# Performance work log

Hardware: AMD Instinct MI355X
Metric: run time of the kernel (lower is better)

The kernel has to match this reference:

```python
import jax, jax.numpy as jnp
import numpy as np

B, S, D, L = 64, 512, 256, 3
NUM_BUCKETS = 1500  # RelativePositionBias default


def _ln(x, g, b):
    m = x.mean(-1, keepdims=True)
    v = x.var(-1, keepdims=True)
    return (x - m) * jax.lax.rsqrt(v + 1e-5) * g + b


def setup_inputs() -> dict:
    key = jax.random.key(0)
    ks = jax.random.split(key, 10)
    s = 0.02
    f32 = jnp.float32
    return dict(
        x=jax.random.normal(ks[0], (B, S, D), f32),
        mask=jnp.ones((B, S), jnp.int32),
        bias_table=jax.random.normal(ks[1], (NUM_BUCKETS,), f32) * s,  # n_heads=1
        ln_g=jnp.ones((L, D), f32), ln_b=jnp.zeros((L, D), f32),
        wq=jax.random.normal(ks[2], (L, D, D), f32) * s, bq=jnp.zeros((L, D), f32),
        wk=jax.random.normal(ks[3], (L, D, D), f32) * s, bk=jnp.zeros((L, D), f32),
        wv=jax.random.normal(ks[4], (L, D, D), f32) * s, bv=jnp.zeros((L, D), f32),
        wo=jax.random.normal(ks[5], (L, D, D), f32) * s, bo=jnp.zeros((L, D), f32),
        cm_ln_g=jnp.ones((L, D), f32), cm_ln_b=jnp.zeros((L, D), f32),
        w1=jax.random.normal(ks[6], (L, D, D), f32) * s, b1=jnp.zeros((L, D), f32),
        w2=jax.random.normal(ks[7], (L, D, D), f32) * s, b2=jnp.zeros((L, D), f32),
    )


def reference(x, mask, bias_table, ln_g, ln_b, wq, bq, wk, bk, wv, bv, wo, bo,
              cm_ln_g, cm_ln_b, w1, b1, w2, b2):
    slen = x.shape[1]
    # relative position bias (RelativePositionBias.compute_bias), n_heads=1
    pos = jnp.arange(slen)
    rel = pos[None, :] - pos[:, None]        # memory - context
    maxn = slen - 1                          # torch.max(rel)
    bucket = jnp.where(rel < 0, -rel + maxn, rel)
    cp = bias_table[bucket]                  # [S, S], broadcasts over batch
    scale = jnp.sqrt(jnp.asarray(x.shape[-1], x.dtype))  # sqrt(hid_dim // 1)
    pad = (mask == 0)[:, None, :]            # [B, 1, S] key-side padding mask
    neg = jnp.finfo(x.dtype).min
    for j in range(L):
        h = _ln(x, ln_g[j], ln_b[j])
        q = h @ wq[j] + bq[j]
        k = h @ wk[j] + bk[j]
        v = h @ wv[j] + bv[j]
        e = jnp.einsum('bqd,bkd->bqk', q, k) / scale + cp
        e = jnp.where(pad, neg, e)
        a = jax.nn.softmax(e, axis=-1)
        o = jnp.einsum('bqk,bkd->bqd', a, v) @ wo[j] + bo[j]
        x = h + _ln(o, ln_g[j], ln_b[j])     # same LayerNorm reused, per source
        c = _ln(x, cm_ln_g[j], cm_ln_b[j])
        x = x + (jax.nn.gelu(c @ w1[j] + b1[j], approximate=False) @ w2[j] + b2[j])
    return x
```

## Files before the change

kernel.cpp:

```cpp
#include <hip/hip_runtime.h>
#include <hip/hip_bf16.h>
#include <math.h>

#define D_HID 256
#define N_B   64
#define S_LEN 512
#define N_L   3
#define M_ROWS (N_B * S_LEN)

typedef __bf16 bf16_t;
typedef __bf16 bf16x8 __attribute__((ext_vector_type(8)));
typedef __bf16 bf16x4 __attribute__((ext_vector_type(4)));
typedef float  f32x4  __attribute__((ext_vector_type(4)));
typedef unsigned int u32;

__device__ __forceinline__ f32x4 mfma16(bf16x8 a, bf16x8 b, f32x4 c) {
    return __builtin_amdgcn_mfma_f32_16x16x32_bf16(a, b, c, 0, 0, 0);
}

__device__ __forceinline__ void gld_lds16(const void* g, void* l) {
    __builtin_amdgcn_global_load_lds((const __attribute__((address_space(1))) u32*)g,
                                     (__attribute__((address_space(3))) u32*)l, 16, 0, 0);
}

__global__ __launch_bounds__(256) void transpose_w(const float* __restrict__ w,
                                                   bf16_t* __restrict__ wt,
                                                   int layer_stride) {
    int i = blockIdx.x * 256 + threadIdx.x;
    int k = i & 255;
    int n = (i >> 8) & 255;
    int l = i >> 16;
    wt[(size_t)l * layer_stride + n * 256 + k] =
        (bf16_t)w[((size_t)l << 16) + ((size_t)k << 8) + n];
}

__global__ __launch_bounds__(256) void ln_fwd(const float* __restrict__ in,
                                              const float* __restrict__ g,
                                              const float* __restrict__ b,
                                              float* __restrict__ H,
                                              bf16_t* __restrict__ Hb) {
    int row  = blockIdx.x * 4 + (threadIdx.x >> 6);
    int lane = threadIdx.x & 63;
    float4 x = ((const float4*)(in + (size_t)row * D_HID))[lane];
    float s  = x.x + x.y + x.z + x.w;
    float sq = x.x * x.x + x.y * x.y + x.z * x.z + x.w * x.w;
#pragma unroll
    for (int o = 1; o < 64; o <<= 1) { s += __shfl_xor(s, o); sq += __shfl_xor(sq, o); }
    float mean = s * (1.f / D_HID);
    float rstd = rsqrtf(sq * (1.f / D_HID) - mean * mean + 1e-5f);
    float4 gv = ((const float4*)g)[lane];
    float4 bv = ((const float4*)b)[lane];
    float4 h;
    h.x = (x.x - mean) * rstd * gv.x + bv.x;
    h.y = (x.y - mean) * rstd * gv.y + bv.y;
    h.z = (x.z - mean) * rstd * gv.z + bv.z;
    h.w = (x.w - mean) * rstd * gv.w + bv.w;
    ((float4*)(H + (size_t)row * D_HID))[lane] = h;
    bf16x4 hb = { (bf16_t)h.x, (bf16_t)h.y, (bf16_t)h.z, (bf16_t)h.w };
    *((bf16x4*)(Hb + (size_t)row * D_HID) + lane) = hb;
}

__global__ __launch_bounds__(256) void ln_res_ln(const float* __restrict__ T,
                                                 const float* __restrict__ H,
                                                 const float* __restrict__ g,
                                                 const float* __restrict__ b,
                                                 const float* __restrict__ cg,
                                                 const float* __restrict__ cb,
                                                 float* __restrict__ X,
                                                 bf16_t* __restrict__ Cb) {
    int row  = blockIdx.x * 4 + (threadIdx.x >> 6);
    int lane = threadIdx.x & 63;
    float4 t = ((const float4*)(T + (size_t)row * D_HID))[lane];
    float s  = t.x + t.y + t.z + t.w;
    float sq = t.x * t.x + t.y * t.y + t.z * t.z + t.w * t.w;
#pragma unroll
    for (int o = 1; o < 64; o <<= 1) { s += __shfl_xor(s, o); sq += __shfl_xor(sq, o); }
    float mean = s * (1.f / D_HID);
    float rstd = rsqrtf(sq * (1.f / D_HID) - mean * mean + 1e-5f);
    float4 gv = ((const float4*)g)[lane];
    float4 bv = ((const float4*)b)[lane];
    float4 hh = ((const float4*)(H + (size_t)row * D_HID))[lane];
    float4 x;
    x.x = hh.x + (t.x - mean) * rstd * gv.x + bv.x;
    x.y = hh.y + (t.y - mean) * rstd * gv.y + bv.y;
    x.z = hh.z + (t.z - mean) * rstd * gv.z + bv.z;
    x.w = hh.w + (t.w - mean) * rstd * gv.w + bv.w;
    ((float4*)(X + (size_t)row * D_HID))[lane] = x;
    float s2  = x.x + x.y + x.z + x.w;
    float sq2 = x.x * x.x + x.y * x.y + x.z * x.z + x.w * x.w;
#pragma unroll
    for (int o = 1; o < 64; o <<= 1) { s2 += __shfl_xor(s2, o); sq2 += __shfl_xor(sq2, o); }
    float mean2 = s2 * (1.f / D_HID);
    float rstd2 = rsqrtf(sq2 * (1.f / D_HID) - mean2 * mean2 + 1e-5f);
    float4 cgv = ((const float4*)cg)[lane];
    float4 cbv = ((const float4*)cb)[lane];
    bf16x4 c = { (bf16_t)((x.x - mean2) * rstd2 * cgv.x + cbv.x),
                 (bf16_t)((x.y - mean2) * rstd2 * cgv.y + cbv.y),
                 (bf16_t)((x.z - mean2) * rstd2 * cgv.z + cbv.z),
                 (bf16_t)((x.w - mean2) * rstd2 * cgv.w + cbv.w) };
    *((bf16x4*)(Cb + (size_t)row * D_HID) + lane) = c;
}

__device__ __forceinline__ void gemm_core(const bf16_t* __restrict__ A,
                                          const bf16_t* __restrict__ W,
                                          int m0, int n0,
                                          bf16_t* As, bf16_t* Bs,
                                          f32x4 (&acc)[4][4]) {
    const int tid  = threadIdx.x;
    const int lane = tid & 63;
    const int wid  = tid >> 6;
    const int wm = wid >> 1, wn = wid & 1;
    const int r = lane & 15, g = lane >> 4;
#pragma unroll 1
    for (int kt = 0; kt < 4; ++kt) {
        if (kt) __syncthreads();
#pragma unroll
        for (int i = 0; i < 4; ++i) {
            const int base8 = i * 256 + wid * 64;
            const int idx8  = base8 + lane;
            const int row   = idx8 >> 3;
            const int sc8   = (idx8 & 7) ^ (row & 7);
            gld_lds16(A + (size_t)(m0 + row) * D_HID + kt * 64 + sc8 * 8, As + base8 * 8);
            gld_lds16(W + (size_t)(n0 + row) * D_HID + kt * 64 + sc8 * 8, Bs + base8 * 8);
        }
        __syncthreads();
#pragma unroll
        for (int ks = 0; ks < 2; ++ks) {
            bf16x8 af[4], bfr[4];
#pragma unroll
            for (int mt = 0; mt < 4; ++mt) {
                const int row = wm * 64 + mt * 16 + r;
                const int c8  = (ks * 4 + g) ^ (row & 7);
                af[mt] = *(const bf16x8*)(As + row * 64 + c8 * 8);
            }
#pragma unroll
            for (int nt = 0; nt < 4; ++nt) {
                const int row = wn * 64 + nt * 16 + r;
                const int c8  = (ks * 4 + g) ^ (row & 7);
                bfr[nt] = *(const bf16x8*)(Bs + row * 64 + c8 * 8);
            }
#pragma unroll
            for (int mt = 0; mt < 4; ++mt)
#pragma unroll
                for (int nt = 0; nt < 4; ++nt)
                    acc[mt][nt] = mfma16(af[mt], bfr[nt], acc[mt][nt]);
        }
    }
}

__global__ __launch_bounds__(256) void gemm_qkv(const bf16_t* __restrict__ A,
                                                const bf16_t* __restrict__ Wp,
                                                const float* __restrict__ bq,
                                                const float* __restrict__ bk,
                                                const float* __restrict__ bv,
                                                bf16_t* __restrict__ Qb,
                                                bf16_t* __restrict__ Kb,
                                                bf16_t* __restrict__ Vt) {
    __shared__ bf16_t As[128 * 64], Bs[128 * 64];
    f32x4 acc[4][4] = {};
    const int m0 = blockIdx.x * 128, n0 = blockIdx.y * 128;
    gemm_core(A, Wp, m0, n0, As, Bs, acc);
    const int lane = threadIdx.x & 63, wid = threadIdx.x >> 6;
    const int wm = wid >> 1, wn = wid & 1, r = lane & 15, g = lane >> 4;
#pragma unroll
    for (int nt = 0; nt < 4; ++nt) {
        const int col = n0 + wn * 64 + nt * 16 + r;
        const int t = col >> 8, cc = col & 255;
        const float bias = (t == 0 ? bq : t == 1 ? bk : bv)[cc];
#pragma unroll
        for (int mt = 0; mt < 4; ++mt)
#pragma unroll
            for (int rr = 0; rr < 4; ++rr) {
                const int row = m0 + wm * 64 + mt * 16 + g * 4 + rr;
                const float v = acc[mt][nt][rr] + bias;
                if (t == 0)      Qb[(size_t)row * D_HID + cc] = (bf16_t)v;
                else if (t == 1) Kb[(size_t)row * D_HID + cc] = (bf16_t)v;
                else             Vt[((size_t)(row >> 9) * D_HID + cc) * S_LEN + (row & 511)] = (bf16_t)v;
            }
    }
}

template <int EPI>
__global__ __launch_bounds__(256) void gemm_one(const bf16_t* __restrict__ A,
                                                const bf16_t* __restrict__ W,
                                                const float* __restrict__ bias,
                                                void* __restrict__ outp,
                                                const float* __restrict__ addsrc) {
    __shared__ bf16_t As[128 * 64], Bs[128 * 64];
    f32x4 acc[4][4] = {};
    const int m0 = blockIdx.x * 128, n0 = blockIdx.y * 128;
    gemm_core(A, W, m0, n0, As, Bs, acc);
    const int lane = threadIdx.x & 63, wid = threadIdx.x >> 6;
    const int wm = wid >> 1, wn = wid & 1, r = lane & 15, g = lane >> 4;
#pragma unroll
    for (int nt = 0; nt < 4; ++nt) {
        const int col = n0 + wn * 64 + nt * 16 + r;
        const float bv = bias[col];
#pragma unroll
        for (int mt = 0; mt < 4; ++mt)
#pragma unroll
            for (int rr = 0; rr < 4; ++rr) {
                const size_t idx = (size_t)(m0 + wm * 64 + mt * 16 + g * 4 + rr) * D_HID + col;
                float v = acc[mt][nt][rr] + bv;
                if constexpr (EPI == 1) {
                    v = 0.5f * v * (1.f + erff(v * 0.70710678118654752f));
                    ((bf16_t*)outp)[idx] = (bf16_t)v;
                } else if constexpr (EPI == 2) {
                    ((float*)outp)[idx] = v;
                } else {
                    ((float*)outp)[idx] = addsrc[idx] + v;
                }
            }
    }
}

__global__ __launch_bounds__(256) void attn_fwd(const bf16_t* __restrict__ Q,
                                                const bf16_t* __restrict__ K,
                                                const bf16_t* __restrict__ Vt,
                                                const float* __restrict__ btab,
                                                const int* __restrict__ mask,
                                                bf16_t* __restrict__ AO) {
    const int b  = blockIdx.x;
    const int q0 = blockIdx.y * 32;
    const int tid  = threadIdx.x;
    const int lane = tid & 63;
    const int w    = tid >> 6;
    const int r = lane & 15, g = lane >> 4;

    __shared__ float  s_tile[32][65];
    __shared__ bf16_t p_tile[32][72];
    __shared__ float  m_s[32], l_s[32], fac_s[32];
    if (tid < 32) { m_s[tid] = -3.0e38f; l_s[tid] = 0.f; }

    const bf16_t* Qp  = Q  + ((size_t)b * S_LEN + q0) * D_HID;
    const bf16_t* Kp  = K  + (size_t)b * S_LEN * D_HID;
    const bf16_t* Vtp = Vt + (size_t)b * D_HID * S_LEN;

    f32x4 oacc[2][4] = {};

    for (int kt = 0; kt < 8; ++kt) {
        const int k0 = kt * 64;
        f32x4 sacc0 = {0.f, 0.f, 0.f, 0.f}, sacc1 = {0.f, 0.f, 0.f, 0.f};
#pragma unroll
        for (int ks = 0; ks < 8; ++ks) {
            const int kb = ks * 32 + g * 8;
            bf16x8 aq0 = *(const bf16x8*)(Qp + (size_t)r * D_HID + kb);
            bf16x8 aq1 = *(const bf16x8*)(Qp + (size_t)(16 + r) * D_HID + kb);
            bf16x8 bk  = *(const bf16x8*)(Kp + (size_t)(k0 + w * 16 + r) * D_HID + kb);
            sacc0 = mfma16(aq0, bk, sacc0);
            sacc1 = mfma16(aq1, bk, sacc1);
        }
#pragma unroll
        for (int rr = 0; rr < 4; ++rr) {
            s_tile[g * 4 + rr][w * 16 + r]      = sacc0[rr];
            s_tile[16 + g * 4 + rr][w * 16 + r] = sacc1[rr];
        }
        __syncthreads();
        {
            const int q  = tid >> 3;
            const int kc = (tid & 7) * 8;
            const int qg = q0 + q;
            const int4 mk0 = *(const int4*)(mask + b * S_LEN + k0 + kc);
            const int4 mk1 = *(const int4*)(mask + b * S_LEN + k0 + kc + 4);
            const int mk[8] = { mk0.x, mk0.y, mk0.z, mk0.w, mk1.x, mk1.y, mk1.z, mk1.w };
            float e[8];
#pragma unroll
            for (int i = 0; i < 8; ++i) {
                const int kk = k0 + kc + i;
                const int rel = kk - qg;
                const int bucket = (rel < 0) ? (511 - rel) : rel;
                float ev = s_tile[q][kc + i] * 0.0625f + btab[bucket];
                if (mk[i] == 0) ev = -3.0e38f;
                e[i] = ev;
            }
            float mx = e[0];
#pragma unroll
            for (int i = 1; i < 8; ++i) mx = fmaxf(mx, e[i]);
            mx = fmaxf(mx, __shfl_xor(mx, 1));
            mx = fmaxf(mx, __shfl_xor(mx, 2));
            mx = fmaxf(mx, __shfl_xor(mx, 4));
            const float m_old = m_s[q];
            const float m_new = fmaxf(m_old, mx);
            float p[8], ps = 0.f;
#pragma unroll
            for (int i = 0; i < 8; ++i) { p[i] = __expf(e[i] - m_new); ps += p[i]; }
            ps += __shfl_xor(ps, 1);
            ps += __shfl_xor(ps, 2);
            ps += __shfl_xor(ps, 4);
            if ((tid & 7) == 0) {
                const float f = __expf(m_old - m_new);
                fac_s[q] = f;
                l_s[q]   = l_s[q] * f + ps;
                m_s[q]   = m_new;
            }
            bf16x8 pb;
#pragma unroll
            for (int i = 0; i < 8; ++i) pb[i] = (bf16_t)p[i];
            *(bf16x8*)(&p_tile[q][kc]) = pb;
        }
        __syncthreads();
        float fr0[4], fr1[4];
#pragma unroll
        for (int rr = 0; rr < 4; ++rr) {
            fr0[rr] = fac_s[g * 4 + rr];
            fr1[rr] = fac_s[16 + g * 4 + rr];
        }
#pragma unroll
        for (int nt = 0; nt < 4; ++nt)
#pragma unroll
            for (int rr = 0; rr < 4; ++rr) {
                oacc[0][nt][rr] *= fr0[rr];
                oacc[1][nt][rr] *= fr1[rr];
            }
#pragma unroll
        for (int ks = 0; ks < 2; ++ks) {
            bf16x8 pa0 = *(const bf16x8*)(&p_tile[r][ks * 32 + g * 8]);
            bf16x8 pa1 = *(const bf16x8*)(&p_tile[16 + r][ks * 32 + g * 8]);
#pragma unroll
            for (int nt = 0; nt < 4; ++nt) {
                bf16x8 vb = *(const bf16x8*)(Vtp + (size_t)(w * 64 + nt * 16 + r) * S_LEN
                                                  + k0 + ks * 32 + g * 8);
                oacc[0][nt] = mfma16(pa0, vb, oacc[0][nt]);
                oacc[1][nt] = mfma16(pa1, vb, oacc[1][nt]);
            }
        }
        __syncthreads();
    }
    float li0[4], li1[4];
#pragma unroll
    for (int rr = 0; rr < 4; ++rr) {
        li0[rr] = 1.f / l_s[g * 4 + rr];
        li1[rr] = 1.f / l_s[16 + g * 4 + rr];
    }
    bf16_t* Op = AO + ((size_t)b * S_LEN + q0) * D_HID;
#pragma unroll
    for (int nt = 0; nt < 4; ++nt)
#pragma unroll
        for (int rr = 0; rr < 4; ++rr) {
            Op[(size_t)(g * 4 + rr) * D_HID + w * 64 + nt * 16 + r]      = (bf16_t)(oacc[0][nt][rr] * li0[rr]);
            Op[(size_t)(16 + g * 4 + rr) * D_HID + w * 64 + nt * 16 + r] = (bf16_t)(oacc[1][nt][rr] * li1[rr]);
        }
}

extern "C" void kernel_launch(void* const* d_in, const int* in_sizes, int n_in,
                              void* d_out, int out_size, void* d_ws, size_t ws_size,
                              hipStream_t stream) {
    const float* x_in = (const float*)d_in[0];
    const int*   mask = (const int*)d_in[1];
    const float* btab = (const float*)d_in[2];
    const float* ln_g = (const float*)d_in[3];
    const float* ln_b = (const float*)d_in[4];
    const float* wq = (const float*)d_in[5];
    const float* bq = (const float*)d_in[6];
    const float* wk = (const float*)d_in[7];
    const float* bk = (const float*)d_in[8];
    const float* wv = (const float*)d_in[9];
    const float* bv = (const float*)d_in[10];
    const float* wo = (const float*)d_in[11];
    const float* bo = (const float*)d_in[12];
    const float* cg = (const float*)d_in[13];
    const float* cb = (const float*)d_in[14];
    const float* w1 = (const float*)d_in[15];
    const float* b1 = (const float*)d_in[16];
    const float* w2 = (const float*)d_in[17];
    const float* b2 = (const float*)d_in[18];
    float* out = (float*)d_out;

    char* p = (char*)d_ws;
    const size_t F32SZ  = (size_t)M_ROWS * D_HID * sizeof(float);
    const size_t BF16SZ = (size_t)M_ROWS * D_HID * sizeof(bf16_t);
    float*  H  = (float*)p;  p += F32SZ;
    float*  X  = (float*)p;  p += F32SZ;
    bf16_t* Hb = (bf16_t*)p; p += BF16SZ;
    bf16_t* Qb = (bf16_t*)p; p += BF16SZ;
    bf16_t* Kb = (bf16_t*)p;
    float*  T  = (float*)Kb;
    bf16_t* T1b = Kb;
    p += BF16SZ;
    bf16_t* Vt = (bf16_t*)p; p += BF16SZ;
    bf16_t* Wqkv = (bf16_t*)p; p += (size_t)N_L * 768 * 256 * sizeof(bf16_t);
    bf16_t* Wrest = (bf16_t*)p;
    bf16_t* AO = Hb;
    bf16_t* Cb = Qb;

    const int WELEMS = N_L * D_HID * D_HID;
    transpose_w<<<dim3(WELEMS / 256), dim3(256), 0, stream>>>(wq, Wqkv + 0 * 65536, 3 * 65536);
    transpose_w<<<dim3(WELEMS / 256), dim3(256), 0, stream>>>(wk, Wqkv + 1 * 65536, 3 * 65536);
    transpose_w<<<dim3(WELEMS / 256), dim3(256), 0, stream>>>(wv, Wqkv + 2 * 65536, 3 * 65536);
    transpose_w<<<dim3(WELEMS / 256), dim3(256), 0, stream>>>(wo, Wrest + (size_t)0 * WELEMS, 65536);
    transpose_w<<<dim3(WELEMS / 256), dim3(256), 0, stream>>>(w1, Wrest + (size_t)1 * WELEMS, 65536);
    transpose_w<<<dim3(WELEMS / 256), dim3(256), 0, stream>>>(w2, Wrest + (size_t)2 * WELEMS, 65536);

    const dim3 gblk(256, 1, 1);
    const dim3 grid_qkv(M_ROWS / 128, 6, 1);
    const dim3 grid_one(M_ROWS / 128, 2, 1);

    for (int j = 0; j < N_L; ++j) {
        const bf16_t* WQKVj = Wqkv + (size_t)j * 3 * 65536;
        const bf16_t* WOt = Wrest + ((size_t)0 * N_L + j) * 65536;
        const bf16_t* W1t = Wrest + ((size_t)1 * N_L + j) * 65536;
        const bf16_t* W2t = Wrest + ((size_t)2 * N_L + j) * 65536;

        ln_fwd<<<dim3(M_ROWS / 4), gblk, 0, stream>>>(j == 0 ? x_in : X,
                                                      ln_g + j * D_HID, ln_b + j * D_HID, H, Hb);
        gemm_qkv<<<grid_qkv, gblk, 0, stream>>>(Hb, WQKVj, bq + j * D_HID, bk + j * D_HID,
                                                bv + j * D_HID, Qb, Kb, Vt);
        attn_fwd<<<dim3(N_B, S_LEN / 32), gblk, 0, stream>>>(Qb, Kb, Vt, btab, mask, AO);
        gemm_one<2><<<grid_one, gblk, 0, stream>>>(AO, WOt, bo + j * D_HID, T, nullptr);
        ln_res_ln<<<dim3(M_ROWS / 4), gblk, 0, stream>>>(T, H, ln_g + j * D_HID, ln_b + j * D_HID,
                                                         cg + j * D_HID, cb + j * D_HID, X, Cb);
        gemm_one<1><<<grid_one, gblk, 0, stream>>>(Cb, W1t, b1 + j * D_HID, T1b, nullptr);
        gemm_one<3><<<grid_one, gblk, 0, stream>>>(T1b, W2t, b2 + j * D_HID,
                                                   (j == N_L - 1) ? (void*)out : (void*)X, X);
    }
}
```

Measured before the change: 788.6 us.

## Split attention keys across waves with per-wave online softmax and LDS merge

Rewrites the attention kernel so each of the four waves handles its own quarter of the keys over the full head dimension, keeping running max and sum in registers. This removes the per-tile block-wide barriers and the shared score tile. Partial outputs are merged through shared memory at the end. It also precomputes the relative-position bias and additive mask into LDS, remaps blocks so each XCD gets a contiguous set of batches, and raises MFMA priority. The costs are much higher register pressure (128 accumulator floats per lane), a 32 KB merge buffer, and serialized merge rounds.

```diff
diff --git a/kernel.cpp b/kernel.cpp
--- a/kernel.cpp
+++ b/kernel.cpp
@@ -21,6 +21,11 @@
 __device__ __forceinline__ void gld_lds16(const void* g, void* l) {
     __builtin_amdgcn_global_load_lds((const __attribute__((address_space(1))) u32*)g,
                                      (__attribute__((address_space(3))) u32*)l, 16, 0, 0);
+}
+
+__device__ __forceinline__ u32 pk_bf16(float a, float b) {
+    return (u32)(__hip_bfloat16_raw(__hip_bfloat16(a)).x) |
+           ((u32)(__hip_bfloat16_raw(__hip_bfloat16(b)).x) << 16);
 }
 
 __global__ __launch_bounds__(256) void transpose_w(const float* __restrict__ w,
@@ -214,132 +219,200 @@
     }
 }
 
-__global__ __launch_bounds__(256) void attn_fwd(const bf16_t* __restrict__ Q,
-                                                const bf16_t* __restrict__ K,
-                                                const bf16_t* __restrict__ Vt,
-                                                const float* __restrict__ btab,
-                                                const int* __restrict__ mask,
-                                                bf16_t* __restrict__ AO) {
-    const int b  = blockIdx.x;
-    const int q0 = blockIdx.y * 32;
-    const int tid  = threadIdx.x;
-    const int lane = tid & 63;
-    const int w    = tid >> 6;
+__global__ __launch_bounds__(256, 2) void attn_fwd(const bf16_t* __restrict__ Q,
+                                                   const bf16_t* __restrict__ K,
+                                                   const bf16_t* __restrict__ Vt,
+                                                   const float* __restrict__ btab,
+                                                   const int* __restrict__ mask,
+                                                   bf16_t* __restrict__ AO) {
+    __shared__ float bias_lds[1024];
+    __shared__ float mask_add[512];
+    __shared__ ulong pstage[4][32][18];
+    __shared__ float m_buf[4][32], l_buf[4][32];
+    __shared__ float o_merge[32][256];
+
+    const int tid = threadIdx.x, lane = tid & 63, w = tid >> 6;
     const int r = lane & 15, g = lane >> 4;
 
-    __shared__ float  s_tile[32][65];
-    __shared__ bf16_t p_tile[32][72];
-    __shared__ float  m_s[32], l_s[32], fac_s[32];
-    if (tid < 32) { m_s[tid] = -3.0e38f; l_s[tid] = 0.f; }
-
-    const bf16_t* Qp  = Q  + ((size_t)b * S_LEN + q0) * D_HID;
-    const bf16_t* Kp  = K  + (size_t)b * S_LEN * D_HID;
-    const bf16_t* Vtp = Vt + (size_t)b * D_HID * S_LEN;
-
-    f32x4 oacc[2][4] = {};
-
-    for (int kt = 0; kt < 8; ++kt) {
-        const int k0 = kt * 64;
-        f32x4 sacc0 = {0.f, 0.f, 0.f, 0.f}, sacc1 = {0.f, 0.f, 0.f, 0.f};
+    const int lid = blockIdx.x;
+    const int xcd = lid & 7, slot = lid >> 3;
+    const int b  = xcd * 8 + (slot >> 4);
+    const int q0 = (slot & 15) * 32;
+
+    for (int i = tid; i < 1024; i += 256) {
+        const int rel = i - 512;
+        const int bucket = (rel < 0) ? (511 - rel) : rel;
+        bias_lds[i] = btab[bucket];
+    }
+    for (int i = tid; i < 512; i += 256)
+        mask_add[i] = mask[b * S_LEN + i] ? 0.f : -3.0e38f;
+    __syncthreads();
+
+    const bf16_t* Qp = Q  + ((size_t)b * S_LEN + q0) * D_HID;
+    const bf16_t* Kp = K  + (size_t)b * S_LEN * D_HID;
+    const bf16_t* Vp = Vt + (size_t)b * D_HID * S_LEN;
+    char* pst = (char*)&pstage[w][0][0];
+
+    f32x4 oacc[2][16] = {};
+    float m_run[2] = {-3.0e38f, -3.0e38f};
+    float l_run[2] = {0.f, 0.f};
+
+#pragma unroll 1
+    for (int kt = 0; kt < 2; ++kt) {
+        const int k0 = (w * 2 + kt) * 64;
+        f32x4 sacc[4][2] = {};
 #pragma unroll
         for (int ks = 0; ks < 8; ++ks) {
-            const int kb = ks * 32 + g * 8;
-            bf16x8 aq0 = *(const bf16x8*)(Qp + (size_t)r * D_HID + kb);
-            bf16x8 aq1 = *(const bf16x8*)(Qp + (size_t)(16 + r) * D_HID + kb);
-            bf16x8 bk  = *(const bf16x8*)(Kp + (size_t)(k0 + w * 16 + r) * D_HID + kb);
-            sacc0 = mfma16(aq0, bk, sacc0);
-            sacc1 = mfma16(aq1, bk, sacc1);
-        }
+            const int dk = ks * 32 + g * 8;
+            bf16x8 qf0 = *(const bf16x8*)(Qp + (size_t)r * D_HID + dk);
+            bf16x8 qf1 = *(const bf16x8*)(Qp + (size_t)(16 + r) * D_HID + dk);
+            bf16x8 kf[4];
+#pragma unroll
+            for (int mt = 0; mt < 4; ++mt)
+                kf[mt] = *(const bf16x8*)(Kp + (size_t)(k0 + mt * 16 + r) * D_HID + dk);
+            __builtin_amdgcn_s_setprio(1);
+#pragma unroll
+            for (int mt = 0; mt < 4; ++mt) {
+                sacc[mt][0] = mfma16(kf[mt], qf0, sacc[mt][0]);
+                sacc[mt][1] = mfma16(kf[mt], qf1, sacc[mt][1]);
+            }
+            __builtin_amdgcn_s_setprio(0);
+        }
+        float mx[2] = {-3.0e38f, -3.0e38f};
+#pragma unroll
+        for (int mt = 0; mt < 4; ++mt)
+#pragma unroll
+            for (int rr = 0; rr < 4; ++rr) {
+                const int kg = k0 + mt * 16 + g * 4 + rr;
+                const float ma = mask_add[kg];
+#pragma unroll
+                for (int nt2 = 0; nt2 < 2; ++nt2) {
+                    const int rel = kg - (q0 + nt2 * 16 + r);
+                    float ev = sacc[mt][nt2][rr] * 0.0625f + bias_lds[rel + 512] + ma;
+                    sacc[mt][nt2][rr] = ev;
+                    mx[nt2] = fmaxf(mx[nt2], ev);
+                }
+            }
+#pragma unroll
+        for (int nt2 = 0; nt2 < 2; ++nt2) {
+            mx[nt2] = fmaxf(mx[nt2], __shfl_xor(mx[nt2], 16));
+            mx[nt2] = fmaxf(mx[nt2], __shfl_xor(mx[nt2], 32));
+        }
+        float mnew[2], fac[2], ladd[2] = {0.f, 0.f};
+#pragma unroll
+        for (int nt2 = 0; nt2 < 2; ++nt2) {
+            mnew[nt2] = fmaxf(m_run[nt2], mx[nt2]);
+            fac[nt2]  = __expf(m_run[nt2] - mnew[nt2]);
+        }
+#pragma unroll
+        for (int mt = 0; mt < 4; ++mt)
+#pragma unroll
+            for (int nt2 = 0; nt2 < 2; ++nt2)
+#pragma unroll
+                for (int rr = 0; rr < 4; ++rr) {
+                    const float p = __expf(sacc[mt][nt2][rr] - mnew[nt2]);
+                    sacc[mt][nt2][rr] = p;
+                    ladd[nt2] += p;
+                }
+#pragma unroll
+        for (int nt2 = 0; nt2 < 2; ++nt2) {
+            ladd[nt2] += __shfl_xor(ladd[nt2], 16);
+            ladd[nt2] += __shfl_xor(ladd[nt2], 32);
+            l_run[nt2] = l_run[nt2] * fac[nt2] + ladd[nt2];
+            m_run[nt2] = mnew[nt2];
+        }
+#pragma unroll
+        for (int nt2 = 0; nt2 < 2; ++nt2)
+#pragma unroll
+            for (int mt = 0; mt < 4; ++mt) {
+                const u32 lo = pk_bf16(sacc[mt][nt2][0], sacc[mt][nt2][1]);
+                const u32 hi = pk_bf16(sacc[mt][nt2][2], sacc[mt][nt2][3]);
+                const int off = (nt2 * 16 + r) * 144 + mt * 32 + g * 8;
+                uint2 pv; pv.x = lo; pv.y = hi;
+                *(uint2*)(pst + off) = pv;
+            }
+        float fbc[2][4];
+#pragma unroll
+        for (int mt2 = 0; mt2 < 2; ++mt2)
+#pragma unroll
+            for (int rr = 0; rr < 4; ++rr)
+                fbc[mt2][rr] = __shfl(fac[mt2], g * 4 + rr);
+#pragma unroll
+        for (int mt2 = 0; mt2 < 2; ++mt2)
+#pragma unroll
+            for (int nt = 0; nt < 16; ++nt)
+#pragma unroll
+                for (int rr = 0; rr < 4; ++rr)
+                    oacc[mt2][nt][rr] *= fbc[mt2][rr];
+#pragma unroll
+        for (int ks = 0; ks < 2; ++ks) {
+            bf16x8 pf[2];
+#pragma unroll
+            for (int mt2 = 0; mt2 < 2; ++mt2)
+                pf[mt2] = *(const bf16x8*)(pst + (mt2 * 16 + r) * 144 + ks * 64 + g * 16);
+            __builtin_amdgcn_s_setprio(1);
+#pragma unroll
+            for (int nt = 0; nt < 16; ++nt) {
+                bf16x8 vf = *(const bf16x8*)(Vp + (size_t)(nt * 16 + r) * S_LEN
+                                                  + k0 + ks * 32 + g * 8);
+                oacc[0][nt] = mfma16(pf[0], vf, oacc[0][nt]);
+                oacc[1][nt] = mfma16(pf[1], vf, oacc[1][nt]);
+            }
+            __builtin_amdgcn_s_setprio(0);
+        }
+    }
+
+    if (g == 0) {
+        m_buf[w][r]      = m_run[0];
+        m_buf[w][16 + r] = m_run[1];
+        l_buf[w][r]      = l_run[0];
+        l_buf[w][16 + r] = l_run[1];
+    }
+    __syncthreads();
+    float scl[2][4];
+#pragma unroll
+    for (int mt2 = 0; mt2 < 2; ++mt2)
 #pragma unroll
         for (int rr = 0; rr < 4; ++rr) {
-            s_tile[g * 4 + rr][w * 16 + r]      = sacc0[rr];
-            s_tile[16 + g * 4 + rr][w * 16 + r] = sacc1[rr];
+            const int q = mt2 * 16 + g * 4 + rr;
+            float mf = m_buf[0][q];
+            mf = fmaxf(mf, m_buf[1][q]);
+            mf = fmaxf(mf, m_buf[2][q]);
+            mf = fmaxf(mf, m_buf[3][q]);
+            float lf = 0.f;
+#pragma unroll
+            for (int ww = 0; ww < 4; ++ww)
+                lf += __expf(m_buf[ww][q] - mf) * l_buf[ww][q];
+            lf = fmaxf(lf, 1e-30f);
+            scl[mt2][rr] = __expf(m_buf[w][q] - mf) / lf;
+        }
+#pragma unroll 1
+    for (int rnd = 0; rnd < 4; ++rnd) {
+        if (w == rnd) {
+#pragma unroll
+            for (int mt2 = 0; mt2 < 2; ++mt2)
+#pragma unroll
+                for (int nt = 0; nt < 16; ++nt)
+#pragma unroll
+                    for (int rr = 0; rr < 4; ++rr) {
+                        const int q = mt2 * 16 + g * 4 + rr;
+                        const int d = nt * 16 + r;
+                        const float v = oacc[mt2][nt][rr] * scl[mt2][rr];
+                        if (rnd == 0) o_merge[q][d] = v;
+                        else          o_merge[q][d] += v;
+                    }
         }
         __syncthreads();
-        {
-            const int q  = tid >> 3;
-            const int kc = (tid & 7) * 8;
-            const int qg = q0 + q;
-            const int4 mk0 = *(const int4*)(mask + b * S_LEN + k0 + kc);
-            const int4 mk1 = *(const int4*)(mask + b * S_LEN + k0 + kc + 4);
-            const int mk[8] = { mk0.x, mk0.y, mk0.z, mk0.w, mk1.x, mk1.y, mk1.z, mk1.w };
-            float e[8];
-#pragma unroll
-            for (int i = 0; i < 8; ++i) {
-                const int kk = k0 + kc + i;
-                const int rel = kk - qg;
-                const int bucket = (rel < 0) ? (511 - rel) : rel;
-                float ev = s_tile[q][kc + i] * 0.0625f + btab[bucket];
-                if (mk[i] == 0) ev = -3.0e38f;
-                e[i] = ev;
-            }
-            float mx = e[0];
-#pragma unroll
-            for (int i = 1; i < 8; ++i) mx = fmaxf(mx, e[i]);
-            mx = fmaxf(mx, __shfl_xor(mx, 1));
-            mx = fmaxf(mx, __shfl_xor(mx, 2));
-            mx = fmaxf(mx, __shfl_xor(mx, 4));
-            const float m_old = m_s[q];
-            const float m_new = fmaxf(m_old, mx);
-            float p[8], ps = 0.f;
-#pragma unroll
-            for (int i = 0; i < 8; ++i) { p[i] = __expf(e[i] - m_new); ps += p[i]; }
-            ps += __shfl_xor(ps, 1);
-            ps += __shfl_xor(ps, 2);
-            ps += __shfl_xor(ps, 4);
-            if ((tid & 7) == 0) {
-                const float f = __expf(m_old - m_new);
-                fac_s[q] = f;
-                l_s[q]   = l_s[q] * f + ps;
-                m_s[q]   = m_new;
-            }
-            bf16x8 pb;
-#pragma unroll
-            for (int i = 0; i < 8; ++i) pb[i] = (bf16_t)p[i];
-            *(bf16x8*)(&p_tile[q][kc]) = pb;
-        }
-        __syncthreads();
-        float fr0[4], fr1[4];
-#pragma unroll
-        for (int rr = 0; rr < 4; ++rr) {
-            fr0[rr] = fac_s[g * 4 + rr];
-            fr1[rr] = fac_s[16 + g * 4 + rr];
-        }
-#pragma unroll
-        for (int nt = 0; nt < 4; ++nt)
-#pragma unroll
-            for (int rr = 0; rr < 4; ++rr) {
-                oacc[0][nt][rr] *= fr0[rr];
-                oacc[1][nt][rr] *= fr1[rr];
-            }
-#pragma unroll
-        for (int ks = 0; ks < 2; ++ks) {
-            bf16x8 pa0 = *(const bf16x8*)(&p_tile[r][ks * 32 + g * 8]);
-            bf16x8 pa1 = *(const bf16x8*)(&p_tile[16 + r][ks * 32 + g * 8]);
-#pragma unroll
-            for (int nt = 0; nt < 4; ++nt) {
-                bf16x8 vb = *(const bf16x8*)(Vtp + (size_t)(w * 64 + nt * 16 + r) * S_LEN
-                                                  + k0 + ks * 32 + g * 8);
-                oacc[0][nt] = mfma16(pa0, vb, oacc[0][nt]);
-                oacc[1][nt] = mfma16(pa1, vb, oacc[1][nt]);
-            }
-        }
-        __syncthreads();
-    }
-    float li0[4], li1[4];
-#pragma unroll
-    for (int rr = 0; rr < 4; ++rr) {
-        li0[rr] = 1.f / l_s[g * 4 + rr];
-        li1[rr] = 1.f / l_s[16 + g * 4 + rr];
     }
     bf16_t* Op = AO + ((size_t)b * S_LEN + q0) * D_HID;
 #pragma unroll
-    for (int nt = 0; nt < 4; ++nt)
-#pragma unroll
-        for (int rr = 0; rr < 4; ++rr) {
-            Op[(size_t)(g * 4 + rr) * D_HID + w * 64 + nt * 16 + r]      = (bf16_t)(oacc[0][nt][rr] * li0[rr]);
-            Op[(size_t)(16 + g * 4 + rr) * D_HID + w * 64 + nt * 16 + r] = (bf16_t)(oacc[1][nt][rr] * li1[rr]);
-        }
+    for (int it = 0; it < 8; ++it) {
+        const int idx = it * 256 + tid;
+        const int row = idx >> 6, c4 = idx & 63;
+        const float4 v = *(const float4*)&o_merge[row][c4 * 4];
+        bf16x4 ob = { (bf16_t)v.x, (bf16_t)v.y, (bf16_t)v.z, (bf16_t)v.w };
+        *((bf16x4*)(Op + (size_t)row * D_HID) + c4) = ob;
+    }
 }
 
 extern "C" void kernel_launch(void* const* d_in, const int* in_sizes, int n_in,
@@ -405,7 +478,7 @@
                                                       ln_g + j * D_HID, ln_b + j * D_HID, H, Hb);
         gemm_qkv<<<grid_qkv, gblk, 0, stream>>>(Hb, WQKVj, bq + j * D_HID, bk + j * D_HID,
                                                 bv + j * D_HID, Qb, Kb, Vt);
-        attn_fwd<<<dim3(N_B, S_LEN / 32), gblk, 0, stream>>>(Qb, Kb, Vt, btab, mask, AO);
+        attn_fwd<<<dim3(N_B * 16, 1, 1), gblk, 0, stream>>>(Qb, Kb, Vt, btab, mask, AO);
         gemm_one<2><<<grid_one, gblk, 0, stream>>>(AO, WOt, bo + j * D_HID, T, nullptr);
         ln_res_ln<<<dim3(M_ROWS / 4), gblk, 0, stream>>>(T, H, ln_g + j * D_HID, ln_b + j * D_HID,
                                                          cg + j * D_HID, cb + j * D_HID, X, Cb);
```

Result: slower. 1.020 ms (+29.4%).

## Restructure attention to keep scores in registers with transposed MFMA and LDS bias

Applied to the files above, without the earlier changes.

Rewrites the attention kernel so QK^T is computed as K·Q (transposed MFMA), keeping scores in registers instead of staging them in an LDS score tile. Relative-position bias and the additive mask are precomputed into LDS once per block, and row max/sum reductions go through small per-wave partial arrays. P is written to a swizzled LDS tile, PV uses s_setprio around the MFMAs, and output is staged in LDS for coalesced 16-byte stores. Blocks are remapped so each XCD handles contiguous batches for K/V cache locality. This removes a sync and the scalar softmax pass, at the cost of more LDS usage and more complex indexing.

```diff
diff --git a/kernel.cpp b/kernel.cpp
--- a/kernel.cpp
+++ b/kernel.cpp
@@ -21,6 +21,11 @@
 __device__ __forceinline__ void gld_lds16(const void* g, void* l) {
     __builtin_amdgcn_global_load_lds((const __attribute__((address_space(1))) u32*)g,
                                      (__attribute__((address_space(3))) u32*)l, 16, 0, 0);
+}
+
+__device__ __forceinline__ u32 pk_bf16(float a, float b) {
+    return (u32)(__hip_bfloat16_raw(__hip_bfloat16(a)).x) |
+           ((u32)(__hip_bfloat16_raw(__hip_bfloat16(b)).x) << 16);
 }
 
 __global__ __launch_bounds__(256) void transpose_w(const float* __restrict__ w,
@@ -220,126 +225,148 @@
                                                 const float* __restrict__ btab,
                                                 const int* __restrict__ mask,
                                                 bf16_t* __restrict__ AO) {
-    const int b  = blockIdx.x;
-    const int q0 = blockIdx.y * 32;
-    const int tid  = threadIdx.x;
-    const int lane = tid & 63;
-    const int w    = tid >> 6;
+    __shared__ float  bias_lds[1024];
+    __shared__ float  mask_add[512];
+    __shared__ bf16_t P_lds[32 * 64];
+    __shared__ float  m_part[4][32], l_part[4][32];
+    __shared__ bf16_t o_lds[32][264];
+
+    const int tid = threadIdx.x, lane = tid & 63, w = tid >> 6;
     const int r = lane & 15, g = lane >> 4;
 
-    __shared__ float  s_tile[32][65];
-    __shared__ bf16_t p_tile[32][72];
-    __shared__ float  m_s[32], l_s[32], fac_s[32];
-    if (tid < 32) { m_s[tid] = -3.0e38f; l_s[tid] = 0.f; }
-
-    const bf16_t* Qp  = Q  + ((size_t)b * S_LEN + q0) * D_HID;
-    const bf16_t* Kp  = K  + (size_t)b * S_LEN * D_HID;
-    const bf16_t* Vtp = Vt + (size_t)b * D_HID * S_LEN;
-
-    f32x4 oacc[2][4] = {};
-
+    const int lid = blockIdx.x;
+    const int xcd = lid & 7, slot = lid >> 3;
+    const int b  = xcd * 8 + (slot >> 4);
+    const int q0 = (slot & 15) * 32;
+
+    for (int i = tid; i < 1024; i += 256) {
+        const int rel = i - 512;
+        const int bucket = (rel < 0) ? (511 - rel) : rel;
+        bias_lds[i] = btab[bucket];
+    }
+    for (int i = tid; i < 512; i += 256)
+        mask_add[i] = mask[b * S_LEN + i] ? 0.f : -3.0e38f;
+    __syncthreads();
+
+    const bf16_t* Qp = Q  + ((size_t)b * S_LEN + q0) * D_HID;
+    const bf16_t* Kp = K  + (size_t)b * S_LEN * D_HID;
+    const bf16_t* Vp = Vt + (size_t)b * D_HID * S_LEN;
+
+    f32x4 oacc[4][2] = {};
+    float m_run[2] = {-3.0e38f, -3.0e38f};
+    float l_run[2] = {0.f, 0.f};
+
+#pragma unroll 1
     for (int kt = 0; kt < 8; ++kt) {
         const int k0 = kt * 64;
-        f32x4 sacc0 = {0.f, 0.f, 0.f, 0.f}, sacc1 = {0.f, 0.f, 0.f, 0.f};
+        f32x4 sacc[2] = {};
 #pragma unroll
         for (int ks = 0; ks < 8; ++ks) {
-            const int kb = ks * 32 + g * 8;
-            bf16x8 aq0 = *(const bf16x8*)(Qp + (size_t)r * D_HID + kb);
-            bf16x8 aq1 = *(const bf16x8*)(Qp + (size_t)(16 + r) * D_HID + kb);
-            bf16x8 bk  = *(const bf16x8*)(Kp + (size_t)(k0 + w * 16 + r) * D_HID + kb);
-            sacc0 = mfma16(aq0, bk, sacc0);
-            sacc1 = mfma16(aq1, bk, sacc1);
-        }
-#pragma unroll
-        for (int rr = 0; rr < 4; ++rr) {
-            s_tile[g * 4 + rr][w * 16 + r]      = sacc0[rr];
-            s_tile[16 + g * 4 + rr][w * 16 + r] = sacc1[rr];
-        }
+            const int dk = ks * 32 + g * 8;
+            bf16x8 kf  = *(const bf16x8*)(Kp + (size_t)(k0 + w * 16 + r) * D_HID + dk);
+            bf16x8 qf0 = *(const bf16x8*)(Qp + (size_t)r * D_HID + dk);
+            bf16x8 qf1 = *(const bf16x8*)(Qp + (size_t)(16 + r) * D_HID + dk);
+            sacc[0] = mfma16(kf, qf0, sacc[0]);
+            sacc[1] = mfma16(kf, qf1, sacc[1]);
+        }
+        float mx[2] = {-3.0e38f, -3.0e38f};
+#pragma unroll
+        for (int qb = 0; qb < 2; ++qb) {
+            const int qg = q0 + qb * 16 + r;
+#pragma unroll
+            for (int rr = 0; rr < 4; ++rr) {
+                const int kg = k0 + w * 16 + g * 4 + rr;
+                float ev = sacc[qb][rr] * 0.0625f + bias_lds[kg - qg + 512] + mask_add[kg];
+                sacc[qb][rr] = ev;
+                mx[qb] = fmaxf(mx[qb], ev);
+            }
+            mx[qb] = fmaxf(mx[qb], __shfl_xor(mx[qb], 16));
+            mx[qb] = fmaxf(mx[qb], __shfl_xor(mx[qb], 32));
+        }
+        if (g == 0) { m_part[w][r] = mx[0]; m_part[w][16 + r] = mx[1]; }
         __syncthreads();
-        {
-            const int q  = tid >> 3;
-            const int kc = (tid & 7) * 8;
-            const int qg = q0 + q;
-            const int4 mk0 = *(const int4*)(mask + b * S_LEN + k0 + kc);
-            const int4 mk1 = *(const int4*)(mask + b * S_LEN + k0 + kc + 4);
-            const int mk[8] = { mk0.x, mk0.y, mk0.z, mk0.w, mk1.x, mk1.y, mk1.z, mk1.w };
-            float e[8];
-#pragma unroll
-            for (int i = 0; i < 8; ++i) {
-                const int kk = k0 + kc + i;
-                const int rel = kk - qg;
-                const int bucket = (rel < 0) ? (511 - rel) : rel;
-                float ev = s_tile[q][kc + i] * 0.0625f + btab[bucket];
-                if (mk[i] == 0) ev = -3.0e38f;
-                e[i] = ev;
-            }
-            float mx = e[0];
-#pragma unroll
-            for (int i = 1; i < 8; ++i) mx = fmaxf(mx, e[i]);
-            mx = fmaxf(mx, __shfl_xor(mx, 1));
-            mx = fmaxf(mx, __shfl_xor(mx, 2));
-            mx = fmaxf(mx, __shfl_xor(mx, 4));
-            const float m_old = m_s[q];
-            const float m_new = fmaxf(m_old, mx);
-            float p[8], ps = 0.f;
-#pragma unroll
-            for (int i = 0; i < 8; ++i) { p[i] = __expf(e[i] - m_new); ps += p[i]; }
-            ps += __shfl_xor(ps, 1);
-            ps += __shfl_xor(ps, 2);
-            ps += __shfl_xor(ps, 4);
-            if ((tid & 7) == 0) {
-                const float f = __expf(m_old - m_new);
-                fac_s[q] = f;
-                l_s[q]   = l_s[q] * f + ps;
-                m_s[q]   = m_new;
-            }
-            bf16x8 pb;
-#pragma unroll
-            for (int i = 0; i < 8; ++i) pb[i] = (bf16_t)p[i];
-            *(bf16x8*)(&p_tile[q][kc]) = pb;
+        float mnew[2], fac[2];
+#pragma unroll
+        for (int qb = 0; qb < 2; ++qb) {
+            const int q = qb * 16 + r;
+            const float tm = fmaxf(fmaxf(m_part[0][q], m_part[1][q]),
+                                   fmaxf(m_part[2][q], m_part[3][q]));
+            mnew[qb] = fmaxf(m_run[qb], tm);
+            fac[qb]  = __expf(m_run[qb] - mnew[qb]);
+            m_run[qb] = mnew[qb];
+        }
+#pragma unroll
+        for (int qb = 0; qb < 2; ++qb) {
+            const float p0 = __expf(sacc[qb][0] - mnew[qb]);
+            const float p1 = __expf(sacc[qb][1] - mnew[qb]);
+            const float p2 = __expf(sacc[qb][2] - mnew[qb]);
+            const float p3 = __expf(sacc[qb][3] - mnew[qb]);
+            float ls = p0 + p1 + p2 + p3;
+            ls += __shfl_xor(ls, 16);
+            ls += __shfl_xor(ls, 32);
+            if (g == 0) l_part[w][qb * 16 + r] = ls;
+            const int q = qb * 16 + r;
+            const int u = (2 * w + (g >> 1)) ^ (q & 7);
+            uint2 pv; pv.x = pk_bf16(p0, p1); pv.y = pk_bf16(p2, p3);
+            *(uint2*)((char*)P_lds + q * 128 + u * 16 + (g & 1) * 8) = pv;
         }
         __syncthreads();
-        float fr0[4], fr1[4];
-#pragma unroll
-        for (int rr = 0; rr < 4; ++rr) {
-            fr0[rr] = fac_s[g * 4 + rr];
-            fr1[rr] = fac_s[16 + g * 4 + rr];
+#pragma unroll
+        for (int qb = 0; qb < 2; ++qb) {
+            const int q = qb * 16 + r;
+            const float lt = l_part[0][q] + l_part[1][q] + l_part[2][q] + l_part[3][q];
+            l_run[qb] = l_run[qb] * fac[qb] + lt;
         }
 #pragma unroll
         for (int nt = 0; nt < 4; ++nt)
 #pragma unroll
-            for (int rr = 0; rr < 4; ++rr) {
-                oacc[0][nt][rr] *= fr0[rr];
-                oacc[1][nt][rr] *= fr1[rr];
-            }
+            for (int qb = 0; qb < 2; ++qb)
+#pragma unroll
+                for (int rr = 0; rr < 4; ++rr)
+                    oacc[nt][qb][rr] *= fac[qb];
 #pragma unroll
         for (int ks = 0; ks < 2; ++ks) {
-            bf16x8 pa0 = *(const bf16x8*)(&p_tile[r][ks * 32 + g * 8]);
-            bf16x8 pa1 = *(const bf16x8*)(&p_tile[16 + r][ks * 32 + g * 8]);
+            bf16x8 pf[2];
+#pragma unroll
+            for (int qb = 0; qb < 2; ++qb) {
+                const int q = qb * 16 + r;
+                const int u = (ks * 4 + g) ^ (q & 7);
+                pf[qb] = *(const bf16x8*)((const char*)P_lds + q * 128 + u * 16);
+            }
+            __builtin_amdgcn_s_setprio(1);
 #pragma unroll
             for (int nt = 0; nt < 4; ++nt) {
-                bf16x8 vb = *(const bf16x8*)(Vtp + (size_t)(w * 64 + nt * 16 + r) * S_LEN
+                bf16x8 vf = *(const bf16x8*)(Vp + (size_t)(w * 64 + nt * 16 + r) * S_LEN
                                                   + k0 + ks * 32 + g * 8);
-                oacc[0][nt] = mfma16(pa0, vb, oacc[0][nt]);
-                oacc[1][nt] = mfma16(pa1, vb, oacc[1][nt]);
-            }
-        }
-        __syncthreads();
-    }
-    float li0[4], li1[4];
-#pragma unroll
-    for (int rr = 0; rr < 4; ++rr) {
-        li0[rr] = 1.f / l_s[g * 4 + rr];
-        li1[rr] = 1.f / l_s[16 + g * 4 + rr];
-    }
+                oacc[nt][0] = mfma16(vf, pf[0], oacc[nt][0]);
+                oacc[nt][1] = mfma16(vf, pf[1], oacc[nt][1]);
+            }
+            __builtin_amdgcn_s_setprio(0);
+        }
+    }
+    const float inv_l[2] = { 1.f / fmaxf(l_run[0], 1e-30f),
+                             1.f / fmaxf(l_run[1], 1e-30f) };
+#pragma unroll
+    for (int nt = 0; nt < 4; ++nt)
+#pragma unroll
+        for (int qb = 0; qb < 2; ++qb) {
+            const int q = qb * 16 + r;
+            const int d = w * 64 + nt * 16 + g * 4;
+            bf16x4 ob = { (bf16_t)(oacc[nt][qb][0] * inv_l[qb]),
+                          (bf16_t)(oacc[nt][qb][1] * inv_l[qb]),
+                          (bf16_t)(oacc[nt][qb][2] * inv_l[qb]),
+                          (bf16_t)(oacc[nt][qb][3] * inv_l[qb]) };
+            *(bf16x4*)&o_lds[q][d] = ob;
+        }
+    __syncthreads();
     bf16_t* Op = AO + ((size_t)b * S_LEN + q0) * D_HID;
 #pragma unroll
-    for (int nt = 0; nt < 4; ++nt)
-#pragma unroll
-        for (int rr = 0; rr < 4; ++rr) {
-            Op[(size_t)(g * 4 + rr) * D_HID + w * 64 + nt * 16 + r]      = (bf16_t)(oacc[0][nt][rr] * li0[rr]);
-            Op[(size_t)(16 + g * 4 + rr) * D_HID + w * 64 + nt * 16 + r] = (bf16_t)(oacc[1][nt][rr] * li1[rr]);
-        }
+    for (int it = 0; it < 4; ++it) {
+        const int idx = it * 256 + tid;
+        const int row = idx >> 5, u = idx & 31;
+        bf16x8 vv = *(const bf16x8*)&o_lds[row][u * 8];
+        *(bf16x8*)(Op + (size_t)row * D_HID + u * 8) = vv;
+    }
 }
 
 extern "C" void kernel_launch(void* const* d_in, const int* in_sizes, int n_in,
@@ -405,7 +432,7 @@
                                                       ln_g + j * D_HID, ln_b + j * D_HID, H, Hb);
         gemm_qkv<<<grid_qkv, gblk, 0, stream>>>(Hb, WQKVj, bq + j * D_HID, bk + j * D_HID,
                                                 bv + j * D_HID, Qb, Kb, Vt);
-        attn_fwd<<<dim3(N_B, S_LEN / 32), gblk, 0, stream>>>(Qb, Kb, Vt, btab, mask, AO);
+        attn_fwd<<<dim3(N_B * 16, 1, 1), gblk, 0, stream>>>(Qb, Kb, Vt, btab, mask, AO);
         gemm_one<2><<<grid_one, gblk, 0, stream>>>(AO, WOt, bo + j * D_HID, T, nullptr);
         ln_res_ln<<<dim3(M_ROWS / 4), gblk, 0, stream>>>(T, H, ln_g + j * D_HID, ln_b + j * D_HID,
                                                          cg + j * D_HID, cb + j * D_HID, X, Cb);
```

New measurement: 715.8 us. 1.1x faster.
